# Optimization experiments

Hardware: AMD Instinct MI355X
Metric: run time of the kernel (lower is better)

The kernel has to match this reference:

```python
import jax, jax.numpy as jnp
import numpy as np

DIM, HID, E, K = 1024, 2048, 8, 2


def setup_inputs() -> dict:
    key = jax.random.key(0)
    ks = jax.random.split(key, 5)
    x = jax.random.normal(ks[0], (2, 2048, DIM), dtype=jnp.float32)
    # router (torch zero-inits; use small random so routing is non-degenerate)
    router_w = jax.random.normal(ks[1], (DIM, E), dtype=jnp.float32) * 0.02
    router_b = jnp.zeros((E,), dtype=jnp.float32)
    # stacked expert params: w12 [E, dim, 2*hidden], w3 [E, hidden, dim]
    w12 = jax.random.normal(ks[2], (E, DIM, 2 * HID), dtype=jnp.float32) * 0.02
    w3 = jax.random.normal(ks[3], (E, HID, DIM), dtype=jnp.float32) * 0.02
    return {"x": x, "router_w": router_w, "router_b": router_b, "w12": w12, "w3": w3}


def reference(x, router_w, router_b, w12, w3):
    # router logits [b, s, e]; eval mode -> no jitter noise
    logits = jnp.einsum("bsd,de->bse", x, router_w) + router_b
    scores = jax.nn.sigmoid(logits)
    top_v, top_i = jax.lax.top_k(scores, K)            # [b, s, k]
    rw = top_v / (jnp.sum(top_v, axis=-1, keepdims=True) + 1e-6)
    # per-token combine weight for each expert (0 if not routed)
    oh = jax.nn.one_hot(top_i, E, dtype=x.dtype)       # [b, s, k, e]
    cw = jnp.einsum("bsk,bske->bse", rw, oh)           # [b, s, e]
    # dense all-expert SwiGLU (matches original masked-dense math)
    x12 = jnp.einsum("bsd,edh->bseh", x, w12)          # [b, s, e, 2H]
    x1, x2 = jnp.split(x12, 2, axis=-1)
    h = jax.nn.silu(x1) * x2                           # [b, s, e, H]
    eout = jnp.einsum("bseh,ehd->bsed", h, w3)         # [b, s, e, dim]
    out = jnp.einsum("bsed,bse->bsd", eout, cw)
    aux_loss = 0.01 * jnp.mean(logits ** 2)
    return out, aux_loss
```

## Files before the change

### kernel.cpp

```cpp
#include <hip/hip_runtime.h>
#include <hip/hip_bf16.h>
#include <stdint.h>

typedef __bf16 bf16_t;
typedef __bf16 bf16x8 __attribute__((ext_vector_type(8)));
typedef __bf16 bf16x4 __attribute__((ext_vector_type(4)));
typedef float f32x4 __attribute__((ext_vector_type(4)));

#define T_TOK 4096
#define DIM   1024
#define HID   2048
#define NE    8

__device__ __forceinline__ void gload_lds16(const void* g, void* l) {
  __builtin_amdgcn_global_load_lds(
      (const __attribute__((address_space(1))) unsigned int*)g,
      (__attribute__((address_space(3))) unsigned int*)l, 16, 0, 0);
}

__global__ __launch_bounds__(256) void k_xconv(const float* __restrict__ x,
                                               bf16_t* __restrict__ xb) {
  int i = (blockIdx.x * 256 + threadIdx.x) * 4;
  float4 v = *(const float4*)(x + i);
  bf16x4 o;
  o[0] = (bf16_t)v.x; o[1] = (bf16_t)v.y; o[2] = (bf16_t)v.z; o[3] = (bf16_t)v.w;
  *(bf16x4*)(xb + i) = o;
}

__global__ __launch_bounds__(256) void k_wt(const float* __restrict__ in,
                                            bf16_t* __restrict__ out,
                                            int K, int N) {
  __shared__ float tile[64][65];
  const size_t eoff = (size_t)blockIdx.z * K * N;
  const int k0 = blockIdx.y * 64, n0 = blockIdx.x * 64;
  const int tid = threadIdx.x;
#pragma unroll
  for (int it = 0; it < 4; ++it) {
    int k = (tid >> 4) + it * 16;
    int n = (tid & 15) * 4;
    float4 v = *(const float4*)(in + eoff + (size_t)(k0 + k) * N + n0 + n);
    tile[k][n] = v.x; tile[k][n + 1] = v.y; tile[k][n + 2] = v.z; tile[k][n + 3] = v.w;
  }
  __syncthreads();
#pragma unroll
  for (int it = 0; it < 2; ++it) {
    int n = (tid >> 3) + it * 32;
    int kc = (tid & 7) * 8;
    bf16x8 o;
#pragma unroll
    for (int j = 0; j < 8; ++j) o[j] = (bf16_t)tile[kc + j][n];
    *(bf16x8*)(out + eoff + (size_t)(n0 + n) * K + k0 + kc) = o;
  }
}

__global__ __launch_bounds__(256) void k_router(const float* __restrict__ x,
    const float* __restrict__ rw, const float* __restrict__ rb,
    int* __restrict__ counts, int* __restrict__ top_i, float* __restrict__ top_w,
    float* __restrict__ aux) {
  int t = blockIdx.x * 4 + (threadIdx.x >> 6);
  int lane = threadIdx.x & 63;
  const float* xt = x + (size_t)t * DIM;
  float acc[8] = {0.f,0.f,0.f,0.f,0.f,0.f,0.f,0.f};
  for (int i = lane; i < DIM; i += 64) {
    float xv = xt[i];
    float4 r0 = *(const float4*)(rw + i * 8);
    float4 r1 = *(const float4*)(rw + i * 8 + 4);
    acc[0] += xv * r0.x; acc[1] += xv * r0.y; acc[2] += xv * r0.z; acc[3] += xv * r0.w;
    acc[4] += xv * r1.x; acc[5] += xv * r1.y; acc[6] += xv * r1.z; acc[7] += xv * r1.w;
  }
#pragma unroll
  for (int m = 32; m >= 1; m >>= 1) {
#pragma unroll
    for (int e = 0; e < 8; ++e) acc[e] += __shfl_xor(acc[e], m, 64);
  }
  if (lane == 0) {
    float s[8]; float sumsq = 0.f;
#pragma unroll
    for (int e = 0; e < 8; ++e) {
      float lg = acc[e] + rb[e];
      sumsq += lg * lg;
      s[e] = 1.f / (1.f + __expf(-lg));
    }
    int i1 = 0;
#pragma unroll
    for (int e = 1; e < 8; ++e) if (s[e] > s[i1]) i1 = e;
    int i2 = (i1 == 0) ? 1 : 0;
#pragma unroll
    for (int e = 0; e < 8; ++e) if (e != i1 && s[e] > s[i2]) i2 = e;
    float v1 = s[i1], v2 = s[i2];
    float den = v1 + v2 + 1e-6f;
    top_i[2 * t]     = i1; top_i[2 * t + 1] = i2;
    top_w[2 * t]     = v1 / den;
    top_w[2 * t + 1] = v2 / den;
    atomicAdd(&counts[i1], 1);
    atomicAdd(&counts[i2], 1);
    atomicAdd(aux, 0.01f * sumsq * (1.f / 32768.f));
  }
}

__global__ void k_scan(const int* __restrict__ counts, int* __restrict__ base) {
  if (threadIdx.x == 0) {
    int s = 0;
    for (int e = 0; e < 8; ++e) { base[e] = s; s += counts[e]; }
  }
}

__global__ __launch_bounds__(256) void k_gather(const int* __restrict__ top_i,
    const float* __restrict__ top_w, const int* __restrict__ base,
    int* __restrict__ fill, int* __restrict__ slot_token, float* __restrict__ slot_wt) {
  int t = blockIdx.x * 256 + threadIdx.x;
  if (t >= T_TOK) return;
#pragma unroll
  for (int j = 0; j < 2; ++j) {
    int e = top_i[2 * t + j];
    int p = atomicAdd(&fill[e], 1);
    int g = base[e] + p;
    slot_token[g] = t;
    slot_wt[g]    = top_w[2 * t + j];
  }
}

__global__ __launch_bounds__(256) void k_gemm1(
    const bf16_t* __restrict__ xb, const bf16_t* __restrict__ w12t,
    const int* __restrict__ counts, const int* __restrict__ base,
    const int* __restrict__ slot_token, bf16_t* __restrict__ h) {
  const int e = blockIdx.z;
  const int cnt = counts[e];
  const int m0 = blockIdx.y * 128;
  if (m0 >= cnt) return;
  const int n0 = blockIdx.x * 64;
  const int bas = base[e];
  const bf16_t* W1 = w12t + (size_t)e * (4096u * 1024u) + (size_t)n0 * 1024u;
  const bf16_t* W2 = W1 + (size_t)2048 * 1024;

  __shared__ bf16_t sA[128 * 64];
  __shared__ bf16_t sB1[64 * 64];
  __shared__ bf16_t sB2[64 * 64];

  const int tid = threadIdx.x, lane = tid & 63, wid = tid >> 6;
  const int wr = wid >> 1, wc = wid & 1;
  const int lr = lane >> 3, sw = (lane & 7) ^ lr;

  int tokA[4];
#pragma unroll
  for (int i = 0; i < 4; ++i) {
    int row = m0 + wid * 32 + i * 8 + lr;
    tokA[i] = slot_token[bas + (row < cnt ? row : cnt - 1)];
  }

  f32x4 acc1[4][2] = {};
  f32x4 acc2[4][2] = {};

  for (int k0 = 0; k0 < DIM; k0 += 64) {
#pragma unroll
    for (int i = 0; i < 4; ++i)
      gload_lds16(xb + (size_t)tokA[i] * DIM + k0 + sw * 8,
                  sA + (wid * 32 + i * 8) * 64);
#pragma unroll
    for (int i = 0; i < 2; ++i) {
      int n = wid * 16 + i * 8 + lr;
      gload_lds16(W1 + (size_t)n * 1024 + k0 + sw * 8, sB1 + (wid * 16 + i * 8) * 64);
      gload_lds16(W2 + (size_t)n * 1024 + k0 + sw * 8, sB2 + (wid * 16 + i * 8) * 64);
    }
    __syncthreads();
#pragma unroll
    for (int kk = 0; kk < 2; ++kk) {
      const int g = kk * 4 + (lane >> 4);
      bf16x8 a[4], b1[2], b2[2];
#pragma unroll
      for (int mf = 0; mf < 4; ++mf) {
        int r = wr * 64 + mf * 16 + (lane & 15);
        a[mf] = *(const bf16x8*)(sA + r * 64 + ((g ^ (r & 7)) << 3));
      }
#pragma unroll
      for (int nf = 0; nf < 2; ++nf) {
        int n = wc * 32 + nf * 16 + (lane & 15);
        b1[nf] = *(const bf16x8*)(sB1 + n * 64 + ((g ^ (n & 7)) << 3));
        b2[nf] = *(const bf16x8*)(sB2 + n * 64 + ((g ^ (n & 7)) << 3));
      }
#pragma unroll
      for (int mf = 0; mf < 4; ++mf)
#pragma unroll
        for (int nf = 0; nf < 2; ++nf) {
          acc1[mf][nf] = __builtin_amdgcn_mfma_f32_16x16x32_bf16(a[mf], b1[nf], acc1[mf][nf], 0, 0, 0);
          acc2[mf][nf] = __builtin_amdgcn_mfma_f32_16x16x32_bf16(a[mf], b2[nf], acc2[mf][nf], 0, 0, 0);
        }
    }
    __syncthreads();
  }
#pragma unroll
  for (int mf = 0; mf < 4; ++mf)
#pragma unroll
    for (int r = 0; r < 4; ++r) {
      int m = wr * 64 + mf * 16 + ((lane >> 4) << 2) + r;
      if (m0 + m < cnt) {
        size_t rowoff = (size_t)(bas + m0 + m) * HID + n0;
#pragma unroll
        for (int nf = 0; nf < 2; ++nf) {
          int col = wc * 32 + nf * 16 + (lane & 15);
          float d1 = acc1[mf][nf][r], d2 = acc2[mf][nf][r];
          h[rowoff + col] = (bf16_t)((d1 / (1.f + __expf(-d1))) * d2);
        }
      }
    }
}

__global__ __launch_bounds__(256) void k_gemm2(
    const bf16_t* __restrict__ h, const bf16_t* __restrict__ w3t,
    const int* __restrict__ counts, const int* __restrict__ base,
    const int* __restrict__ slot_token, const float* __restrict__ slot_wt,
    float* __restrict__ out) {
  const int e = blockIdx.z;
  const int cnt = counts[e];
  const int m0 = blockIdx.y * 128;
  if (m0 >= cnt) return;
  const int n0 = blockIdx.x * 128;
  const int bas = base[e];
  const bf16_t* W = w3t + (size_t)e * (1024u * 2048u);

  __shared__ bf16_t sA[128 * 64];
  __shared__ bf16_t sB[128 * 64];

  const int tid = threadIdx.x, lane = tid & 63, wid = tid >> 6;
  const int wr = wid >> 1, wc = wid & 1;
  const int lr = lane >> 3, sw = (lane & 7) ^ lr;

  int rowA[4];
#pragma unroll
  for (int i = 0; i < 4; ++i) {
    int row = m0 + wid * 32 + i * 8 + lr;
    rowA[i] = bas + (row < cnt ? row : cnt - 1);
  }

  f32x4 acc[4][4] = {};

  for (int k0 = 0; k0 < HID; k0 += 64) {
#pragma unroll
    for (int i = 0; i < 4; ++i) {
      gload_lds16(h + (size_t)rowA[i] * HID + k0 + sw * 8,
                  sA + (wid * 32 + i * 8) * 64);
      int n = wid * 32 + i * 8 + lr;
      gload_lds16(W + (size_t)(n0 + n) * 2048 + k0 + sw * 8,
                  sB + (wid * 32 + i * 8) * 64);
    }
    __syncthreads();
#pragma unroll
    for (int kk = 0; kk < 2; ++kk) {
      const int g = kk * 4 + (lane >> 4);
      bf16x8 a[4], b[4];
#pragma unroll
      for (int mf = 0; mf < 4; ++mf) {
        int r = wr * 64 + mf * 16 + (lane & 15);
        a[mf] = *(const bf16x8*)(sA + r * 64 + ((g ^ (r & 7)) << 3));
      }
#pragma unroll
      for (int nf = 0; nf < 4; ++nf) {
        int n = wc * 64 + nf * 16 + (lane & 15);
        b[nf] = *(const bf16x8*)(sB + n * 64 + ((g ^ (n & 7)) << 3));
      }
#pragma unroll
      for (int mf = 0; mf < 4; ++mf)
#pragma unroll
        for (int nf = 0; nf < 4; ++nf)
          acc[mf][nf] = __builtin_amdgcn_mfma_f32_16x16x32_bf16(a[mf], b[nf], acc[mf][nf], 0, 0, 0);
    }
    __syncthreads();
  }
#pragma unroll
  for (int mf = 0; mf < 4; ++mf)
#pragma unroll
    for (int r = 0; r < 4; ++r) {
      int m = wr * 64 + mf * 16 + ((lane >> 4) << 2) + r;
      if (m0 + m < cnt) {
        int gs = bas + m0 + m;
        int tok = slot_token[gs];
        float wt = slot_wt[gs];
        size_t o = (size_t)tok * DIM + n0;
#pragma unroll
        for (int nf = 0; nf < 4; ++nf) {
          int col = wc * 64 + nf * 16 + (lane & 15);
          atomicAdd(out + o + col, acc[mf][nf][r] * wt);
        }
      }
    }
}

extern "C" void kernel_launch(void* const* d_in, const int* in_sizes, int n_in,
                              void* d_out, int out_size, void* d_ws, size_t ws_size,
                              hipStream_t stream) {
  const float* x   = (const float*)d_in[0];
  const float* rw  = (const float*)d_in[1];
  const float* rb  = (const float*)d_in[2];
  const float* w12 = (const float*)d_in[3];
  const float* w3  = (const float*)d_in[4];
  float* out = (float*)d_out;

  char* ws = (char*)d_ws;
  int*   counts     = (int*)(ws + 0);
  int*   fill       = (int*)(ws + 64);
  int*   base       = (int*)(ws + 128);
  int*   top_i      = (int*)(ws + 4096);
  float* top_w      = (float*)(ws + 4096 + 32768);
  int*   slot_token = (int*)(ws + 4096 + 65536);
  float* slot_wt    = (float*)(ws + 4096 + 98304);
  bf16_t* xb        = (bf16_t*)(ws + 262144);
  bf16_t* h         = (bf16_t*)(ws + 262144 + 8388608);
  bf16_t* wT        = (bf16_t*)(ws + 262144 + 8388608 + 33554432);

  hipMemsetAsync(d_out, 0, (size_t)out_size * sizeof(float), stream);
  hipMemsetAsync(ws, 0, 256, stream);

  k_xconv<<<dim3(T_TOK * DIM / 4 / 256), dim3(256), 0, stream>>>(x, xb);
  k_wt<<<dim3(64, 16, NE), dim3(256), 0, stream>>>(w12, wT, DIM, 2 * HID);
  k_router<<<dim3(T_TOK / 4), dim3(256), 0, stream>>>(x, rw, rb, counts, top_i, top_w,
                                                      out + (size_t)T_TOK * DIM);
  k_scan<<<dim3(1), dim3(64), 0, stream>>>(counts, base);
  k_gather<<<dim3(T_TOK / 256), dim3(256), 0, stream>>>(top_i, top_w, base, fill,
                                                        slot_token, slot_wt);
  k_gemm1<<<dim3(HID / 64, T_TOK / 128, NE), dim3(256), 0, stream>>>(
      xb, wT, counts, base, slot_token, h);
  k_wt<<<dim3(16, 32, NE), dim3(256), 0, stream>>>(w3, wT, HID, DIM);
  k_gemm2<<<dim3(DIM / 128, T_TOK / 128, NE), dim3(256), 0, stream>>>(
      h, wT, counts, base, slot_token, slot_wt, out);
}
```

Measured before the change: 416.8 us.

## Compact MoE tile grid, fuse x conversion into router, replace atomics with combine

Folds the fp32-to-bf16 conversion of x into the router kernel, so x is read once and one launch goes away. A planning kernel builds a compact list of (expert, m0) tiles, so the grouped GEMMs launch only about 72 row tiles instead of 8x32 blocks that mostly exit early. GEMM2 now writes weighted per-slot outputs in bf16 instead of doing fp32 atomicAdds into out, and a new combine kernel sums each token's two slots. This also removes the full output memset, at the cost of an extra bf16 intermediate buffer, an extra kernel, and bf16 rounding of the partial outputs.

Result: faster. 399.3 us (-4.2%).

```diff
diff --git a/kernel.cpp b/kernel.cpp
--- a/kernel.cpp
+++ b/kernel.cpp
@@ -11,20 +11,12 @@
 #define DIM   1024
 #define HID   2048
 #define NE    8
+#define MAXT  72
 
 __device__ __forceinline__ void gload_lds16(const void* g, void* l) {
   __builtin_amdgcn_global_load_lds(
       (const __attribute__((address_space(1))) unsigned int*)g,
       (__attribute__((address_space(3))) unsigned int*)l, 16, 0, 0);
-}
-
-__global__ __launch_bounds__(256) void k_xconv(const float* __restrict__ x,
-                                               bf16_t* __restrict__ xb) {
-  int i = (blockIdx.x * 256 + threadIdx.x) * 4;
-  float4 v = *(const float4*)(x + i);
-  bf16x4 o;
-  o[0] = (bf16_t)v.x; o[1] = (bf16_t)v.y; o[2] = (bf16_t)v.z; o[3] = (bf16_t)v.w;
-  *(bf16x4*)(xb + i) = o;
 }
 
 __global__ __launch_bounds__(256) void k_wt(const float* __restrict__ in,
@@ -56,17 +48,26 @@
 __global__ __launch_bounds__(256) void k_router(const float* __restrict__ x,
     const float* __restrict__ rw, const float* __restrict__ rb,
     int* __restrict__ counts, int* __restrict__ top_i, float* __restrict__ top_w,
-    float* __restrict__ aux) {
+    float* __restrict__ aux, bf16_t* __restrict__ xb) {
   int t = blockIdx.x * 4 + (threadIdx.x >> 6);
   int lane = threadIdx.x & 63;
   const float* xt = x + (size_t)t * DIM;
   float acc[8] = {0.f,0.f,0.f,0.f,0.f,0.f,0.f,0.f};
-  for (int i = lane; i < DIM; i += 64) {
-    float xv = xt[i];
-    float4 r0 = *(const float4*)(rw + i * 8);
-    float4 r1 = *(const float4*)(rw + i * 8 + 4);
-    acc[0] += xv * r0.x; acc[1] += xv * r0.y; acc[2] += xv * r0.z; acc[3] += xv * r0.w;
-    acc[4] += xv * r1.x; acc[5] += xv * r1.y; acc[6] += xv * r1.z; acc[7] += xv * r1.w;
+#pragma unroll
+  for (int it = 0; it < 4; ++it) {
+    int i = (it * 64 + lane) * 4;
+    float4 xv = *(const float4*)(xt + i);
+    bf16x4 o;
+    o[0] = (bf16_t)xv.x; o[1] = (bf16_t)xv.y; o[2] = (bf16_t)xv.z; o[3] = (bf16_t)xv.w;
+    *(bf16x4*)(xb + (size_t)t * DIM + i) = o;
+#pragma unroll
+    for (int c = 0; c < 4; ++c) {
+      float v = (c == 0) ? xv.x : (c == 1) ? xv.y : (c == 2) ? xv.z : xv.w;
+      float4 r0 = *(const float4*)(rw + (size_t)(i + c) * 8);
+      float4 r1 = *(const float4*)(rw + (size_t)(i + c) * 8 + 4);
+      acc[0] += v * r0.x; acc[1] += v * r0.y; acc[2] += v * r0.z; acc[3] += v * r0.w;
+      acc[4] += v * r1.x; acc[5] += v * r1.y; acc[6] += v * r1.z; acc[7] += v * r1.w;
+    }
   }
 #pragma unroll
   for (int m = 32; m >= 1; m >>= 1) {
@@ -98,16 +99,24 @@
   }
 }
 
-__global__ void k_scan(const int* __restrict__ counts, int* __restrict__ base) {
+__global__ void k_plan(const int* __restrict__ counts, int* __restrict__ base,
+                       int* __restrict__ tile_e, int* __restrict__ tile_m0) {
   if (threadIdx.x == 0) {
-    int s = 0;
-    for (int e = 0; e < 8; ++e) { base[e] = s; s += counts[e]; }
+    int s = 0, nt = 0;
+    for (int e = 0; e < NE; ++e) {
+      base[e] = s;
+      int c = counts[e];
+      for (int m0 = 0; m0 < c; m0 += 128) { tile_e[nt] = e; tile_m0[nt] = m0; ++nt; }
+      s += c;
+    }
+    for (; nt < MAXT; ++nt) tile_e[nt] = -1;
   }
 }
 
 __global__ __launch_bounds__(256) void k_gather(const int* __restrict__ top_i,
     const float* __restrict__ top_w, const int* __restrict__ base,
-    int* __restrict__ fill, int* __restrict__ slot_token, float* __restrict__ slot_wt) {
+    int* __restrict__ fill, int* __restrict__ slot_token, float* __restrict__ slot_wt,
+    int* __restrict__ slot_of) {
   int t = blockIdx.x * 256 + threadIdx.x;
   if (t >= T_TOK) return;
 #pragma unroll
@@ -117,19 +126,21 @@
     int g = base[e] + p;
     slot_token[g] = t;
     slot_wt[g]    = top_w[2 * t + j];
+    slot_of[2 * t + j] = g;
   }
 }
 
 __global__ __launch_bounds__(256) void k_gemm1(
     const bf16_t* __restrict__ xb, const bf16_t* __restrict__ w12t,
     const int* __restrict__ counts, const int* __restrict__ base,
+    const int* __restrict__ tile_e, const int* __restrict__ tile_m0,
     const int* __restrict__ slot_token, bf16_t* __restrict__ h) {
-  const int e = blockIdx.z;
+  const int e = tile_e[blockIdx.y];
+  if (e < 0) return;
+  const int m0  = tile_m0[blockIdx.y];
   const int cnt = counts[e];
-  const int m0 = blockIdx.y * 128;
-  if (m0 >= cnt) return;
+  const int bas = base[e];
   const int n0 = blockIdx.x * 64;
-  const int bas = base[e];
   const bf16_t* W1 = w12t + (size_t)e * (4096u * 1024u) + (size_t)n0 * 1024u;
   const bf16_t* W2 = W1 + (size_t)2048 * 1024;
 
@@ -208,14 +219,14 @@
 __global__ __launch_bounds__(256) void k_gemm2(
     const bf16_t* __restrict__ h, const bf16_t* __restrict__ w3t,
     const int* __restrict__ counts, const int* __restrict__ base,
-    const int* __restrict__ slot_token, const float* __restrict__ slot_wt,
-    float* __restrict__ out) {
-  const int e = blockIdx.z;
+    const int* __restrict__ tile_e, const int* __restrict__ tile_m0,
+    const float* __restrict__ slot_wt, bf16_t* __restrict__ eout) {
+  const int e = tile_e[blockIdx.y];
+  if (e < 0) return;
+  const int m0  = tile_m0[blockIdx.y];
   const int cnt = counts[e];
-  const int m0 = blockIdx.y * 128;
-  if (m0 >= cnt) return;
+  const int bas = base[e];
   const int n0 = blockIdx.x * 128;
-  const int bas = base[e];
   const bf16_t* W = w3t + (size_t)e * (1024u * 2048u);
 
   __shared__ bf16_t sA[128 * 64];
@@ -273,16 +284,30 @@
       int m = wr * 64 + mf * 16 + ((lane >> 4) << 2) + r;
       if (m0 + m < cnt) {
         int gs = bas + m0 + m;
-        int tok = slot_token[gs];
         float wt = slot_wt[gs];
-        size_t o = (size_t)tok * DIM + n0;
+        size_t o = (size_t)gs * DIM + n0;
 #pragma unroll
         for (int nf = 0; nf < 4; ++nf) {
           int col = wc * 64 + nf * 16 + (lane & 15);
-          atomicAdd(out + o + col, acc[mf][nf][r] * wt);
+          eout[o + col] = (bf16_t)(acc[mf][nf][r] * wt);
         }
       }
     }
+}
+
+__global__ __launch_bounds__(256) void k_combine(const bf16_t* __restrict__ eout,
+    const int* __restrict__ slot_of, float* __restrict__ out) {
+  const int t = blockIdx.x;
+  const int c = threadIdx.x * 4;
+  const int g0 = slot_of[2 * t], g1 = slot_of[2 * t + 1];
+  bf16x4 a = *(const bf16x4*)(eout + (size_t)g0 * DIM + c);
+  bf16x4 b = *(const bf16x4*)(eout + (size_t)g1 * DIM + c);
+  float4 o;
+  o.x = (float)a[0] + (float)b[0];
+  o.y = (float)a[1] + (float)b[1];
+  o.z = (float)a[2] + (float)b[2];
+  o.w = (float)a[3] + (float)b[3];
+  *(float4*)(out + (size_t)t * DIM + c) = o;
 }
 
 extern "C" void kernel_launch(void* const* d_in, const int* in_sizes, int n_in,
@@ -294,6 +319,7 @@
   const float* w12 = (const float*)d_in[3];
   const float* w3  = (const float*)d_in[4];
   float* out = (float*)d_out;
+  float* aux = out + (size_t)T_TOK * DIM;
 
   char* ws = (char*)d_ws;
   int*   counts     = (int*)(ws + 0);
@@ -303,23 +329,27 @@
   float* top_w      = (float*)(ws + 4096 + 32768);
   int*   slot_token = (int*)(ws + 4096 + 65536);
   float* slot_wt    = (float*)(ws + 4096 + 98304);
+  int*   slot_of    = (int*)(ws + 4096 + 131072);
+  int*   tile_e     = (int*)(ws + 4096 + 163840);
+  int*   tile_m0    = (int*)(ws + 4096 + 164352);
   bf16_t* xb        = (bf16_t*)(ws + 262144);
   bf16_t* h         = (bf16_t*)(ws + 262144 + 8388608);
   bf16_t* wT        = (bf16_t*)(ws + 262144 + 8388608 + 33554432);
-
-  hipMemsetAsync(d_out, 0, (size_t)out_size * sizeof(float), stream);
+  bf16_t* eout      = (bf16_t*)((char*)wT + 33554432);
+
   hipMemsetAsync(ws, 0, 256, stream);
-
-  k_xconv<<<dim3(T_TOK * DIM / 4 / 256), dim3(256), 0, stream>>>(x, xb);
+  hipMemsetAsync(aux, 0, sizeof(float), stream);
+
   k_wt<<<dim3(64, 16, NE), dim3(256), 0, stream>>>(w12, wT, DIM, 2 * HID);
   k_router<<<dim3(T_TOK / 4), dim3(256), 0, stream>>>(x, rw, rb, counts, top_i, top_w,
-                                                      out + (size_t)T_TOK * DIM);
-  k_scan<<<dim3(1), dim3(64), 0, stream>>>(counts, base);
+                                                      aux, xb);
+  k_plan<<<dim3(1), dim3(64), 0, stream>>>(counts, base, tile_e, tile_m0);
   k_gather<<<dim3(T_TOK / 256), dim3(256), 0, stream>>>(top_i, top_w, base, fill,
-                                                        slot_token, slot_wt);
-  k_gemm1<<<dim3(HID / 64, T_TOK / 128, NE), dim3(256), 0, stream>>>(
-      xb, wT, counts, base, slot_token, h);
+                                                        slot_token, slot_wt, slot_of);
+  k_gemm1<<<dim3(HID / 64, MAXT), dim3(256), 0, stream>>>(
+      xb, wT, counts, base, tile_e, tile_m0, slot_token, h);
   k_wt<<<dim3(16, 32, NE), dim3(256), 0, stream>>>(w3, wT, HID, DIM);
-  k_gemm2<<<dim3(DIM / 128, T_TOK / 128, NE), dim3(256), 0, stream>>>(
-      h, wT, counts, base, slot_token, slot_wt, out);
-}
+  k_gemm2<<<dim3(DIM / 128, MAXT), dim3(256), 0, stream>>>(
+      h, wT, counts, base, tile_e, tile_m0, slot_wt, eout);
+  k_combine<<<dim3(T_TOK), dim3(256), 0, stream>>>(eout, slot_of, out);
+}
```
